# Kernel optimization log

Hardware: AMD Instinct MI355X
Metric: run time of the kernel (lower is better)

Reference implementation:

```python
import jax, jax.numpy as jnp
import numpy as np

N = 1_000_000   # total elements
G = 100_000     # number of groups (all guaranteed non-empty)
D = 128         # emb_dim


def setup_inputs() -> dict:
    key = jax.random.key(0)
    k1, k2, k3, k4, k5, k6 = jax.random.split(key, 6)
    embeddings = jax.random.normal(k1, (N, D), dtype=jnp.float32)
    # sorted segment ids with every id in [0, G) present at least once
    extra = jax.random.randint(k2, (N - G,), 0, G, dtype=jnp.int32)
    seg_ids = jnp.sort(jnp.concatenate([jnp.arange(G, dtype=jnp.int32), extra]))
    # nn.Linear default init: U(-1/sqrt(fan_in), 1/sqrt(fan_in))
    s = 1.0 / np.sqrt(D)
    Wq = jax.random.uniform(k3, (D, D), jnp.float32, -s, s)
    bq = jax.random.uniform(k4, (D,), jnp.float32, -s, s)
    Wk = jax.random.uniform(k5, (D, D), jnp.float32, -s, s)
    bk = jax.random.uniform(k6, (D,), jnp.float32, -s, s)
    return {"embeddings": embeddings, "seg_ids": seg_ids,
            "Wq": Wq, "bq": bq, "Wk": Wk, "bk": bk}


def reference(embeddings, seg_ids, Wq, bq, Wk, bk):
    # keys = key_layer(embeddings), computed once for all elements  [N, D]
    keys = embeddings @ Wk.T + bk
    # index of the LAST element of each (sorted, contiguous) segment
    counts = jax.ops.segment_sum(jnp.ones_like(seg_ids), seg_ids, num_segments=G)
    last_idx = jnp.cumsum(counts) - 1                       # [G]
    # query = query_layer(group_emb[-1])                    [G, D]
    q = embeddings[last_idx] @ Wq.T + bq
    # per-element attention logit: <q[group(i)], keys[i]>   [N]
    logits = jnp.sum(q[seg_ids] * keys, axis=-1)
    # segment-wise stable softmax
    m = jax.ops.segment_max(logits, seg_ids, num_segments=G)
    e = jnp.exp(logits - m[seg_ids])
    denom = jax.ops.segment_sum(e, seg_ids, num_segments=G)
    w = e / denom[seg_ids]                                  # [N]
    # weighted sum of keys per segment                      [G, D]
    out = jax.ops.segment_sum(w[:, None] * keys, seg_ids, num_segments=G)
    return out
```

## Files before the change

kernel.cpp:

```cpp
#include <hip/hip_runtime.h>
#include <math.h>

typedef _Float16 half8  __attribute__((ext_vector_type(8)));
typedef _Float16 half2v __attribute__((ext_vector_type(2)));
typedef float    floatx4 __attribute__((ext_vector_type(4)));

#define LGKM_FENCE() asm volatile("s_waitcnt lgkmcnt(0)" ::: "memory")

__global__ void seg_bounds_kernel(const int* __restrict__ seg,
                                  int* __restrict__ seg_start, int N, int G) {
    int i = blockIdx.x * 256 + threadIdx.x;
    if (i >= N) return;
    int s = seg[i];
    if (i == 0 || s != seg[i - 1]) seg_start[s] = i;
    if (i == N - 1) seg_start[G] = N;
}

__device__ inline half8 pack8(float4 a, float4 b) {
    half8 r;
    r[0] = (_Float16)a.x; r[1] = (_Float16)a.y; r[2] = (_Float16)a.z; r[3] = (_Float16)a.w;
    r[4] = (_Float16)b.x; r[5] = (_Float16)b.y; r[6] = (_Float16)b.z; r[7] = (_Float16)b.w;
    return r;
}

__global__ __launch_bounds__(64, 2) void fused_attn_kernel(
    const float* __restrict__ emb, const int* __restrict__ seg_start,
    const float* __restrict__ Wq, const float* __restrict__ bq,
    const float* __restrict__ Wk, const float* __restrict__ bk,
    float* __restrict__ out)
{
    __shared__ alignas(16) _Float16 keys_lds[16][136];
    __shared__ alignas(16) _Float16 q_lds[8][136];
    __shared__ alignas(16) float    L_lds[16];

    const int lane = threadIdx.x;
    const int m    = lane & 15;
    const int quad = lane >> 4;

    const int g0 = blockIdx.x * 8;
    const int s0 = seg_start[g0];
    const int e0 = seg_start[g0 + 8];

    int sb[9];
#pragma unroll
    for (int i = 0; i <= 8; ++i) sb[i] = seg_start[g0 + i];

    float bkv[8];
#pragma unroll
    for (int c = 0; c < 8; ++c) bkv[c] = bk[16 * c + m];

    {
        int  qm   = (m < 8) ? m : 7;
        long qrow = (long)seg_start[g0 + qm + 1] - 1;
        half8 aq[4];
#pragma unroll
        for (int kq = 0; kq < 4; ++kq) {
            const float4* p = (const float4*)(emb + qrow * 128 + kq * 32 + quad * 8);
            aq[kq] = pack8(p[0], p[1]);
        }
#pragma unroll
        for (int c = 0; c < 8; ++c) {
            float bqc = bq[16 * c + m];
            floatx4 acc = {bqc, bqc, bqc, bqc};
#pragma unroll
            for (int kq = 0; kq < 4; ++kq) {
                const float4* wp = (const float4*)(Wq + (16 * c + m) * 128 + kq * 32 + quad * 8);
                half8 bf = pack8(wp[0], wp[1]);
                acc = __builtin_amdgcn_mfma_f32_16x16x32_f16(aq[kq], bf, acc, 0, 0, 0);
            }
            if (quad < 2) {
#pragma unroll
                for (int r = 0; r < 4; ++r)
                    q_lds[quad * 4 + r][16 * c + m] = (_Float16)acc[r];
            }
        }
    }
    LGKM_FENCE();

    half8 wkf[8][4];
#pragma unroll
    for (int c = 0; c < 8; ++c)
#pragma unroll
        for (int kq = 0; kq < 4; ++kq) {
            const float4* wp = (const float4*)(Wk + (16 * c + m) * 128 + kq * 32 + quad * 8);
            wkf[c][kq] = pack8(wp[0], wp[1]);
        }

    const int nt = (e0 - s0 + 15) >> 4;

    float4 pre[8];
    {
        long prow = (long)min(s0 + m, e0 - 1);
#pragma unroll
        for (int kq = 0; kq < 4; ++kq) {
            const float4* p = (const float4*)(emb + prow * 128 + kq * 32 + quad * 8);
            pre[2 * kq] = p[0]; pre[2 * kq + 1] = p[1];
        }
    }

    int   g = g0;
    int   cur_end = sb[1];
    float run_m = -INFINITY, run_d = 0.f, acc0 = 0.f, acc1 = 0.f;

    for (int tt = 0; tt < nt; ++tt) {
        const int t   = s0 + tt * 16;
        const int cnt = min(16, e0 - t);

        half8 ak[4];
#pragma unroll
        for (int kq = 0; kq < 4; ++kq)
            ak[kq] = pack8(pre[2 * kq], pre[2 * kq + 1]);

        if (tt + 1 < nt) {
            long nrow = (long)min(t + 16 + m, e0 - 1);
#pragma unroll
            for (int kq = 0; kq < 4; ++kq) {
                const float4* p = (const float4*)(emb + nrow * 128 + kq * 32 + quad * 8);
                pre[2 * kq] = p[0]; pre[2 * kq + 1] = p[1];
            }
        }

#pragma unroll
        for (int c = 0; c < 8; ++c) {
            floatx4 acc = {bkv[c], bkv[c], bkv[c], bkv[c]};
#pragma unroll
            for (int kq = 0; kq < 4; ++kq)
                acc = __builtin_amdgcn_mfma_f32_16x16x32_f16(ak[kq], wkf[c][kq], acc, 0, 0, 0);
#pragma unroll
            for (int r = 0; r < 4; ++r)
                keys_lds[quad * 4 + r][16 * c + m] = (_Float16)acc[r];
        }
        LGKM_FENCE();

        floatx4 lacc = {0.f, 0.f, 0.f, 0.f};
#pragma unroll
        for (int kq = 0; kq < 4; ++kq) {
            half8 af = *(const half8*)&keys_lds[m][kq * 32 + quad * 8];
            half8 bf = *(const half8*)&q_lds[m & 7][kq * 32 + quad * 8];
            lacc = __builtin_amdgcn_mfma_f32_16x16x32_f16(af, bf, lacc, 0, 0, 0);
        }
#pragma unroll
        for (int r = 0; r < 4; ++r) {
            int rowc = min(t + quad * 4 + r, e0 - 1);
            int sl = 0;
#pragma unroll
            for (int i = 1; i < 8; ++i) sl += (rowc >= sb[i]) ? 1 : 0;
            if (m == sl) L_lds[quad * 4 + r] = lacc[r];
        }
        LGKM_FENCE();

        float lg[16];
#pragma unroll
        for (int i = 0; i < 4; ++i) {
            float4 v = *(const float4*)&L_lds[4 * i];
            lg[4 * i] = v.x; lg[4 * i + 1] = v.y; lg[4 * i + 2] = v.z; lg[4 * i + 3] = v.w;
        }
        half2v kv[16];
#pragma unroll
        for (int r = 0; r < 16; ++r)
            kv[r] = *(const half2v*)&keys_lds[r][2 * lane];

#pragma unroll
        for (int rl = 0; rl < 16; ++rl) {
            if (rl < cnt) {
                int row = t + rl;
                while (row >= cur_end) {
                    float inv = 1.0f / run_d;
                    float2 o; o.x = acc0 * inv; o.y = acc1 * inv;
                    *(float2*)(out + (long)g * 128 + 2 * lane) = o;
                    ++g;
                    cur_end = seg_start[g + 1];
                    run_m = -INFINITY; run_d = 0.f; acc0 = 0.f; acc1 = 0.f;
                }
                float logit = lg[rl];
                float k0 = (float)kv[rl][0], k1 = (float)kv[rl][1];
                float nm = fmaxf(run_m, logit);
                float sc = __expf(run_m - nm);
                float e  = __expf(logit - nm);
                run_d = run_d * sc + e;
                acc0  = acc0 * sc + e * k0;
                acc1  = acc1 * sc + e * k1;
                run_m = nm;
            }
        }
    }
    {
        float inv = 1.0f / run_d;
        float2 o; o.x = acc0 * inv; o.y = acc1 * inv;
        *(float2*)(out + (long)g * 128 + 2 * lane) = o;
    }
}

extern "C" void kernel_launch(void* const* d_in, const int* in_sizes, int n_in,
                              void* d_out, int out_size, void* d_ws, size_t ws_size,
                              hipStream_t stream) {
    const float* emb = (const float*)d_in[0];
    const int*   seg = (const int*)d_in[1];
    const float* Wq  = (const float*)d_in[2];
    const float* bq  = (const float*)d_in[3];
    const float* Wk  = (const float*)d_in[4];
    const float* bk  = (const float*)d_in[5];
    float* out = (float*)d_out;

    const int N = in_sizes[1];
    const int G = out_size / 128;

    int* seg_start = (int*)d_ws;

    seg_bounds_kernel<<<(N + 255) / 256, 256, 0, stream>>>(seg, seg_start, N, G);
    fused_attn_kernel<<<G / 8, 64, 0, stream>>>(emb, seg_start, Wq, bq, Wk, bk, out);
}
```

Baseline: 803.4 us.

## Replace serial per-row online softmax with MFMA segment-weighted accumulation over 16 groups

```diff
diff --git a/kernel.cpp b/kernel.cpp
--- a/kernel.cpp
+++ b/kernel.cpp
@@ -2,10 +2,11 @@
 #include <math.h>
 
 typedef _Float16 half8  __attribute__((ext_vector_type(8)));
-typedef _Float16 half2v __attribute__((ext_vector_type(2)));
+typedef _Float16 half4  __attribute__((ext_vector_type(4)));
 typedef float    floatx4 __attribute__((ext_vector_type(4)));
 
 #define LGKM_FENCE() asm volatile("s_waitcnt lgkmcnt(0)" ::: "memory")
+#define NEG_INF (-__builtin_inff())
 
 __global__ void seg_bounds_kernel(const int* __restrict__ seg,
                                   int* __restrict__ seg_start, int N, int G) {
@@ -23,35 +24,49 @@
     return r;
 }
 
+__device__ inline float bperm(float v, int srcLane) {
+    return __int_as_float(__builtin_amdgcn_ds_bpermute(srcLane * 4, __float_as_int(v)));
+}
+
 __global__ __launch_bounds__(64, 2) void fused_attn_kernel(
     const float* __restrict__ emb, const int* __restrict__ seg_start,
     const float* __restrict__ Wq, const float* __restrict__ bq,
     const float* __restrict__ Wk, const float* __restrict__ bk,
     float* __restrict__ out)
 {
-    __shared__ alignas(16) _Float16 keys_lds[16][136];
-    __shared__ alignas(16) _Float16 q_lds[8][136];
+    __shared__ alignas(16) _Float16 keys_lds[16][152];
+    __shared__ alignas(16) _Float16 q_lds[16][152];
     __shared__ alignas(16) float    L_lds[16];
 
     const int lane = threadIdx.x;
     const int m    = lane & 15;
     const int quad = lane >> 4;
 
-    const int g0 = blockIdx.x * 8;
+    const int g0 = blockIdx.x * 16;
     const int s0 = seg_start[g0];
-    const int e0 = seg_start[g0 + 8];
-
-    int sb[9];
-#pragma unroll
-    for (int i = 0; i <= 8; ++i) sb[i] = seg_start[g0 + i];
+    const int e0 = seg_start[g0 + 16];
+
+    const int sbm  = seg_start[g0 + m];
+    const int sbm1 = seg_start[g0 + m + 1];
 
     float bkv[8];
 #pragma unroll
     for (int c = 0; c < 8; ++c) bkv[c] = bk[16 * c + m];
 
+    const int nt = (e0 - s0 + 15) >> 4;
+
+    float4 pre[8];
     {
-        int  qm   = (m < 8) ? m : 7;
-        long qrow = (long)seg_start[g0 + qm + 1] - 1;
+        long prow = (long)min(s0 + m, e0 - 1);
+#pragma unroll
+        for (int kq = 0; kq < 4; ++kq) {
+            const float4* p = (const float4*)(emb + prow * 128 + kq * 32 + quad * 8);
+            pre[2 * kq] = p[0]; pre[2 * kq + 1] = p[1];
+        }
+    }
+
+    {
+        long qrow = (long)seg_start[g0 + m + 1] - 1;
         half8 aq[4];
 #pragma unroll
         for (int kq = 0; kq < 4; ++kq) {
@@ -68,14 +83,11 @@
                 half8 bf = pack8(wp[0], wp[1]);
                 acc = __builtin_amdgcn_mfma_f32_16x16x32_f16(aq[kq], bf, acc, 0, 0, 0);
             }
-            if (quad < 2) {
-#pragma unroll
-                for (int r = 0; r < 4; ++r)
-                    q_lds[quad * 4 + r][16 * c + m] = (_Float16)acc[r];
-            }
-        }
-    }
-    LGKM_FENCE();
+#pragma unroll
+            for (int r = 0; r < 4; ++r)
+                q_lds[quad * 4 + r][16 * c + m] = (_Float16)acc[r];
+        }
+    }
 
     half8 wkf[8][4];
 #pragma unroll
@@ -86,30 +98,25 @@
             wkf[c][kq] = pack8(wp[0], wp[1]);
         }
 
-    const int nt = (e0 - s0 + 15) >> 4;
-
-    float4 pre[8];
-    {
-        long prow = (long)min(s0 + m, e0 - 1);
-#pragma unroll
-        for (int kq = 0; kq < 4; ++kq) {
-            const float4* p = (const float4*)(emb + prow * 128 + kq * 32 + quad * 8);
-            pre[2 * kq] = p[0]; pre[2 * kq + 1] = p[1];
-        }
-    }
-
-    int   g = g0;
-    int   cur_end = sb[1];
-    float run_m = -INFINITY, run_d = 0.f, acc0 = 0.f, acc1 = 0.f;
+    LGKM_FENCE();
+
+    half8 ak_next[4];
+#pragma unroll
+    for (int kq = 0; kq < 4; ++kq)
+        ak_next[kq] = pack8(pre[2 * kq], pre[2 * kq + 1]);
+
+    floatx4 acc8[8];
+#pragma unroll
+    for (int c = 0; c < 8; ++c) acc8[c] = (floatx4){0.f, 0.f, 0.f, 0.f};
+
+    float run_m = NEG_INF, run_d = 0.f;
 
     for (int tt = 0; tt < nt; ++tt) {
-        const int t   = s0 + tt * 16;
-        const int cnt = min(16, e0 - t);
+        const int t = s0 + tt * 16;
 
         half8 ak[4];
 #pragma unroll
-        for (int kq = 0; kq < 4; ++kq)
-            ak[kq] = pack8(pre[2 * kq], pre[2 * kq + 1]);
+        for (int kq = 0; kq < 4; ++kq) ak[kq] = ak_next[kq];
 
         if (tt + 1 < nt) {
             long nrow = (long)min(t + 16 + m, e0 - 1);
@@ -120,15 +127,20 @@
             }
         }
 
+        half4 keysB[8];
 #pragma unroll
         for (int c = 0; c < 8; ++c) {
-            floatx4 acc = {bkv[c], bkv[c], bkv[c], bkv[c]};
+            floatx4 kacc = {bkv[c], bkv[c], bkv[c], bkv[c]};
 #pragma unroll
             for (int kq = 0; kq < 4; ++kq)
-                acc = __builtin_amdgcn_mfma_f32_16x16x32_f16(ak[kq], wkf[c][kq], acc, 0, 0, 0);
+                kacc = __builtin_amdgcn_mfma_f32_16x16x32_f16(ak[kq], wkf[c][kq], kacc, 0, 0, 0);
 #pragma unroll
             for (int r = 0; r < 4; ++r)
-                keys_lds[quad * 4 + r][16 * c + m] = (_Float16)acc[r];
+                keys_lds[quad * 4 + r][16 * c + m] = (_Float16)kacc[r];
+            half4 kb;
+            kb[0] = (_Float16)kacc[0]; kb[1] = (_Float16)kacc[1];
+            kb[2] = (_Float16)kacc[2]; kb[3] = (_Float16)kacc[3];
+            keysB[c] = kb;
         }
         LGKM_FENCE();
 
@@ -136,16 +148,13 @@
 #pragma unroll
         for (int kq = 0; kq < 4; ++kq) {
             half8 af = *(const half8*)&keys_lds[m][kq * 32 + quad * 8];
-            half8 bf = *(const half8*)&q_lds[m & 7][kq * 32 + quad * 8];
+            half8 bf = *(const half8*)&q_lds[m][kq * 32 + quad * 8];
             lacc = __builtin_amdgcn_mfma_f32_16x16x32_f16(af, bf, lacc, 0, 0, 0);
         }
 #pragma unroll
         for (int r = 0; r < 4; ++r) {
             int rowc = min(t + quad * 4 + r, e0 - 1);
-            int sl = 0;
-#pragma unroll
-            for (int i = 1; i < 8; ++i) sl += (rowc >= sb[i]) ? 1 : 0;
-            if (m == sl) L_lds[quad * 4 + r] = lacc[r];
+            if (rowc >= sbm && rowc < sbm1) L_lds[quad * 4 + r] = lacc[r];
         }
         LGKM_FENCE();
 
@@ -155,39 +164,80 @@
             float4 v = *(const float4*)&L_lds[4 * i];
             lg[4 * i] = v.x; lg[4 * i + 1] = v.y; lg[4 * i + 2] = v.z; lg[4 * i + 3] = v.w;
         }
-        half2v kv[16];
-#pragma unroll
-        for (int r = 0; r < 16; ++r)
-            kv[r] = *(const half2v*)&keys_lds[r][2 * lane];
-
-#pragma unroll
-        for (int rl = 0; rl < 16; ++rl) {
-            if (rl < cnt) {
-                int row = t + rl;
-                while (row >= cur_end) {
-                    float inv = 1.0f / run_d;
-                    float2 o; o.x = acc0 * inv; o.y = acc1 * inv;
-                    *(float2*)(out + (long)g * 128 + 2 * lane) = o;
-                    ++g;
-                    cur_end = seg_start[g + 1];
-                    run_m = -INFINITY; run_d = 0.f; acc0 = 0.f; acc1 = 0.f;
-                }
-                float logit = lg[rl];
-                float k0 = (float)kv[rl][0], k1 = (float)kv[rl][1];
-                float nm = fmaxf(run_m, logit);
-                float sc = __expf(run_m - nm);
-                float e  = __expf(logit - nm);
-                run_d = run_d * sc + e;
-                acc0  = acc0 * sc + e * k0;
-                acc1  = acc1 * sc + e * k1;
-                run_m = nm;
-            }
-        }
-    }
-    {
-        float inv = 1.0f / run_d;
-        float2 o; o.x = acc0 * inv; o.y = acc1 * inv;
-        *(float2*)(out + (long)g * 128 + 2 * lane) = o;
+
+        float lgz[16];
+        bool  cnd[16];
+#pragma unroll
+        for (int r = 0; r < 16; ++r) {
+            int row = t + r;
+            cnd[r] = (row >= sbm) && (row < sbm1);
+            lgz[r] = cnd[r] ? lg[r] : NEG_INF;
+        }
+        float mx8[8], mx4[4], mx2[2], tm;
+#pragma unroll
+        for (int i = 0; i < 8; ++i) mx8[i] = fmaxf(lgz[2 * i], lgz[2 * i + 1]);
+#pragma unroll
+        for (int i = 0; i < 4; ++i) mx4[i] = fmaxf(mx8[2 * i], mx8[2 * i + 1]);
+        mx2[0] = fmaxf(mx4[0], mx4[1]); mx2[1] = fmaxf(mx4[2], mx4[3]);
+        tm = fmaxf(mx2[0], mx2[1]);
+
+        bool  upd = tm > run_m;
+        float sc  = upd ? __expf(run_m - tm) : 1.0f;
+        float nm  = upd ? tm : run_m;
+
+        float ez[16];
+#pragma unroll
+        for (int r = 0; r < 16; ++r) {
+            float e = __expf(lg[r] - nm);
+            ez[r] = cnd[r] ? e : 0.f;
+        }
+        float s8[8], s4[4], s2[2];
+#pragma unroll
+        for (int i = 0; i < 8; ++i) s8[i] = ez[2 * i] + ez[2 * i + 1];
+#pragma unroll
+        for (int i = 0; i < 4; ++i) s4[i] = s8[2 * i] + s8[2 * i + 1];
+        s2[0] = s4[0] + s4[1]; s2[1] = s4[2] + s4[3];
+        run_d = fmaf(run_d, sc, s2[0] + s2[1]);
+        run_m = nm;
+
+        float scr[4];
+#pragma unroll
+        for (int reg = 0; reg < 4; ++reg)
+            scr[reg] = bperm(sc, quad * 4 + reg);
+#pragma unroll
+        for (int c = 0; c < 8; ++c) {
+            acc8[c][0] *= scr[0]; acc8[c][1] *= scr[1];
+            acc8[c][2] *= scr[2]; acc8[c][3] *= scr[3];
+        }
+
+        half4 afr;
+#pragma unroll
+        for (int j = 0; j < 4; ++j) {
+            float v = (quad == 0) ? ez[j] : (quad == 1) ? ez[4 + j]
+                    : (quad == 2) ? ez[8 + j] : ez[12 + j];
+            afr[j] = (_Float16)v;
+        }
+#pragma unroll
+        for (int c = 0; c < 8; ++c)
+            acc8[c] = __builtin_amdgcn_mfma_f32_16x16x16f16(afr, keysB[c], acc8[c], 0, 0, 0);
+
+        if (tt + 1 < nt) {
+#pragma unroll
+            for (int kq = 0; kq < 4; ++kq)
+                ak_next[kq] = pack8(pre[2 * kq], pre[2 * kq + 1]);
+        }
+    }
+
+    float dinv[4];
+#pragma unroll
+    for (int reg = 0; reg < 4; ++reg)
+        dinv[reg] = __builtin_amdgcn_rcpf(bperm(run_d, quad * 4 + reg));
+#pragma unroll
+    for (int reg = 0; reg < 4; ++reg) {
+        long orow = (long)(g0 + quad * 4 + reg) * 128;
+#pragma unroll
+        for (int c = 0; c < 8; ++c)
+            out[orow + 16 * c + m] = acc8[c][reg] * dinv[reg];
     }
 }
 
@@ -208,5 +258,5 @@
     int* seg_start = (int*)d_ws;
 
     seg_bounds_kernel<<<(N + 255) / 256, 256, 0, stream>>>(seg, seg_start, N, G);
-    fused_attn_kernel<<<G / 8, 64, 0, stream>>>(emb, seg_start, Wq, bq, Wk, bk, out);
-}
+    fused_attn_kernel<<<G / 16, 64, 0, stream>>>(emb, seg_start, Wq, bq, Wk, bk, out);
+}
```

After: 953.3 us. 1.19x slower.
